# Kernel tuning notes

Hardware: AMD Instinct MI355X
Metric: run time of the kernel (lower is better)

The kernel has to match this reference:

```python
import jax, jax.numpy as jnp
import numpy as np

EPS = 1e-5
SLOPE = 0.2


def setup_inputs() -> dict:
    key = jax.random.key(0)
    ks = jax.random.split(key, 8)
    B, D, N = 8, 60, 1024
    dims = [(64, 120), (64, 64), (128, 64), (256, 128), (256, 512), (1024, 256)]
    inp = {"x": jax.random.normal(ks[0], (B, D, N), dtype=jnp.float32)}
    for i, (o, c) in enumerate(dims, 1):
        inp[f"w{i}"] = jax.random.normal(ks[i], (o, c), dtype=jnp.float32) / np.sqrt(c).astype(np.float32)
        inp[f"b{i}"] = jnp.zeros((o,), jnp.float32)
        inp[f"g{i}"] = jnp.ones((o,), jnp.float32)
        inp[f"be{i}"] = jnp.zeros((o,), jnp.float32)
    inp["k"] = 20
    return inp


def knn_idx(x, k):
    # x: [B, D, N] -> idx [B, N, k] of nearest neighbors (negative sq dist topk)
    inner = -2.0 * jnp.einsum('bdn,bdm->bnm', x, x)
    xx = jnp.sum(x * x, axis=1)  # [B, N]
    pd = -xx[:, :, None] - inner - xx[:, None, :]
    _, idx = jax.lax.top_k(pd, k)
    return idx


def get_graph_feature(x, k):
    # x: [B, D, N] -> [B, 2D, N, k]
    B, D, N = x.shape
    idx = knn_idx(x, k)  # [B, N, k]
    xt = jnp.transpose(x, (0, 2, 1))  # [B, N, D]
    nbr = xt[jnp.arange(B)[:, None, None], idx]  # [B, N, k, D]
    ctr = xt[:, :, None, :]  # [B, N, 1, D]
    feat = jnp.concatenate([nbr - ctr, jnp.broadcast_to(ctr, nbr.shape)], axis=-1)
    return jnp.transpose(feat, (0, 3, 1, 2))  # [B, 2D, N, k]


def lrelu(x):
    return jnp.where(x >= 0, x, SLOPE * x)


def bn(x, g, b, axes):
    # training-mode batch norm (biased variance), channel axis = 1
    m = jnp.mean(x, axis=axes, keepdims=True)
    v = jnp.mean((x - m) ** 2, axis=axes, keepdims=True)
    sh = [1] * x.ndim
    sh[1] = -1
    return (x - m) * jax.lax.rsqrt(v + EPS) * g.reshape(sh) + b.reshape(sh)


def conv2d1x1(x, w, b):
    return jnp.einsum('bcnk,oc->bonk', x, w) + b[None, :, None, None]


def conv1d1x1(x, w, b):
    return jnp.einsum('bcn,oc->bon', x, w) + b[None, :, None]


def reference(x, w1, b1, g1, be1, w2, b2, g2, be2, w3, b3, g3, be3,
              w4, b4, g4, be4, w5, b5, g5, be5, w6, b6, g6, be6, k):
    h = get_graph_feature(x, k)                             # [B,120,N,k]
    h = lrelu(bn(conv2d1x1(h, w1, b1), g1, be1, (0, 2, 3)))
    x1 = jnp.max(h, axis=-1)
    h = lrelu(bn(conv2d1x1(h, w2, b2), g2, be2, (0, 2, 3)))
    x2 = jnp.max(h, axis=-1)
    h = lrelu(bn(conv2d1x1(h, w3, b3), g3, be3, (0, 2, 3)))
    x3 = jnp.max(h, axis=-1)
    h = lrelu(bn(conv2d1x1(h, w4, b4), g4, be4, (0, 2, 3)))
    x4 = jnp.max(h, axis=-1)
    h = jnp.concatenate([x1, x2, x3, x4], axis=1)           # [B,512,N]
    h = lrelu(bn(conv1d1x1(h, w5, b5), g5, be5, (0, 2)))
    h = lrelu(bn(conv1d1x1(h, w6, b6), g6, be6, (0, 2)))
    return jnp.transpose(h, (0, 2, 1))                      # [B,N,emb_dims]
```

## Files before the change

kernel.cpp:

```cpp
#include <hip/hip_runtime.h>
#include <hip/hip_bf16.h>
#include <math.h>

#define B_ 8
#define D_ 60
#define N_ 1024
#define K_ 20
#define P1_ 8192
#define P2_ 163840

typedef __attribute__((ext_vector_type(8))) short bf16x8;
typedef __attribute__((ext_vector_type(4))) short bf16x4;
typedef __attribute__((ext_vector_type(4))) float f32x4;

__device__ inline float b2f(short s) { return __uint_as_float(((unsigned)(unsigned short)s) << 16); }
__device__ inline short f2b(float f) { __hip_bfloat16 h = __float2bfloat16(f); return *(short*)&h; }
__device__ inline unsigned fenc(float f) { unsigned b = __float_as_uint(f); return (b & 0x80000000u) ? ~b : (b | 0x80000000u); }
__device__ inline float fdec(unsigned k) { return __uint_as_float((k & 0x80000000u) ? (k ^ 0x80000000u) : ~k); }

#define OFF_IDX   0ull
#define OFF_XX    655360ull
#define OFF_STATS 688128ull
#define OFF_XT    720896ull
#define OFF_WB    1769472ull
#define OFF_XC    2662400ull
#define OFF_H5    11051008ull
#define OFF_H6    15245312ull
#define OFF_UV    32022528ull
#define OFF_XR1   36216832ull
#define OFF_XR2   38313984ull
#define OFF_XR3   40411136ull
#define OFF_XR4   44605440ull
#define OFF_H1    52994048ull
#define OFF_H2    73965568ull
#define OFF_H3    94937088ull
#define OFF_PART  136880128ull
#define OFF_PART2 139501568ull

#define WO1 0
#define WO2 8192
#define WO3 12288
#define WO4 20480
#define WO5 53248
#define WO6 184320

#define SO1 0
#define SO2 64
#define SO3 128
#define SO4 256
#define SO5 512
#define SO6 768
#define NCH_TOT 1792

__global__ __launch_bounds__(256) void k_xx(const float* __restrict__ x,
                                            float* __restrict__ xx) {
  int bn = blockIdx.x * 256 + threadIdx.x;
  int b = bn >> 10, n = bn & 1023;
  const float* xb = x + (size_t)b * D_ * N_ + n;
  float s = 0.f;
  for (int d = 0; d < D_; ++d) { float v = xb[(size_t)d * N_]; s += v * v; }
  xx[bn] = s;
}

__global__ __launch_bounds__(256) void k_pd(const float* __restrict__ x,
                                            const float* __restrict__ xx,
                                            float* __restrict__ pd) {
  __shared__ float lnn[D_][64];
  __shared__ float lmm[D_][128];
  int tid = threadIdx.x;
  int m0 = blockIdx.x * 128, n0 = blockIdx.y * 64, b = blockIdx.z;
  const float* xb = x + (size_t)b * D_ * N_;
  #pragma unroll
  for (int i = 0; i < 15; ++i) {
    int idx = tid + i * 256;
    int d = idx >> 6, col = idx & 63;
    lnn[d][col] = xb[(size_t)d * N_ + n0 + col];
  }
  #pragma unroll
  for (int i = 0; i < 30; ++i) {
    int idx = tid + i * 256;
    int d = idx >> 7, col = idx & 127;
    lmm[d][col] = xb[(size_t)d * N_ + m0 + col];
  }
  __syncthreads();
  int tn = tid >> 5, tm = tid & 31;
  float acc[8][4];
  #pragma unroll
  for (int i = 0; i < 8; ++i)
    #pragma unroll
    for (int j = 0; j < 4; ++j) acc[i][j] = 0.f;
  for (int d = 0; d < D_; ++d) {
    f32x4 mv  = *(const f32x4*)&lmm[d][tm * 4];
    f32x4 nva = *(const f32x4*)&lnn[d][tn * 8];
    f32x4 nvb = *(const f32x4*)&lnn[d][tn * 8 + 4];
    #pragma unroll
    for (int i = 0; i < 4; ++i)
      #pragma unroll
      for (int j = 0; j < 4; ++j) {
        acc[i][j]     = fmaf(nva[i], mv[j], acc[i][j]);
        acc[4 + i][j] = fmaf(nvb[i], mv[j], acc[4 + i][j]);
      }
  }
  const float* xxb = xx + b * 1024;
  f32x4 xxm = *(const f32x4*)(xxb + m0 + tm * 4);
  #pragma unroll
  for (int i = 0; i < 8; ++i) {
    int n = n0 + tn * 8 + i;
    float xxn = xxb[n];
    f32x4 o;
    #pragma unroll
    for (int j = 0; j < 4; ++j) o[j] = 2.f * acc[i][j] - xxn - xxm[j];
    *(f32x4*)(pd + ((size_t)(b * 1024 + n) * 1024) + m0 + tm * 4) = o;
  }
}

__global__ __launch_bounds__(256) void k_sel(const float* __restrict__ pd,
                                             int* __restrict__ idxb) {
  int tid = threadIdx.x;
  int wave = tid >> 6, lane = tid & 63;
  int bn = blockIdx.x * 4 + wave;
  const float* row = pd + (size_t)bn * 1024;
  int mbase = lane * 16;
  f32x4 r0 = *(const f32x4*)(row + mbase);
  f32x4 r1 = *(const f32x4*)(row + mbase + 4);
  f32x4 r2 = *(const f32x4*)(row + mbase + 8);
  f32x4 r3 = *(const f32x4*)(row + mbase + 12);
  float v[16];
  #pragma unroll
  for (int j = 0; j < 4; ++j) { v[j] = r0[j]; v[4 + j] = r1[j]; v[8 + j] = r2[j]; v[12 + j] = r3[j]; }
  int* outp = idxb + (size_t)bn * K_;
  for (int kk = 0; kk < K_; ++kk) {
    float bv = v[0]; int bj = 0;
    #pragma unroll
    for (int j = 1; j < 16; ++j)
      if (v[j] > bv) { bv = v[j]; bj = j; }
    int bi = mbase + bj;
    #pragma unroll
    for (int off = 1; off < 64; off <<= 1) {
      float ov = __shfl_xor(bv, off);
      int   oi = __shfl_xor(bi, off);
      if (ov > bv || (ov == bv && oi < bi)) { bv = ov; bi = oi; }
    }
    if (lane == 0) outp[kk] = bi;
    #pragma unroll
    for (int j = 0; j < 16; ++j)
      if (bi == mbase + j) v[j] = -INFINITY;
  }
}

__global__ __launch_bounds__(256) void k_xt(const float* __restrict__ x,
                                            short* __restrict__ xt) {
  int bn = blockIdx.x * 256 + threadIdx.x;
  int b = bn >> 10, n = bn & 1023;
  const float* xb = x + (size_t)b * D_ * N_ + n;
  short* row = xt + (size_t)bn * 64;
  for (int c = 0; c < 60; ++c) row[c] = f2b(xb[(size_t)c * N_]);
  row[60] = 0; row[61] = 0; row[62] = 0; row[63] = 0;
}

__global__ __launch_bounds__(256) void k_wuv(const float* __restrict__ w1,
                                             const float* __restrict__ b1,
                                             short* __restrict__ wuv,
                                             float* __restrict__ buv) {
  int t = blockIdx.x * 256 + threadIdx.x;
  int o = t >> 6, c = t & 63;
  float v = 0.f;
  if (o < 64) { if (c < 60) v = w1[o * 120 + c]; }
  else { int o2 = o - 64; if (c < 60) v = w1[o2 * 120 + 60 + c] - w1[o2 * 120 + c]; }
  wuv[t] = f2b(v);
  if (t < 128) buv[t] = (t < 64) ? 0.f : b1[t - 64];
}

__global__ __launch_bounds__(256) void k_wcvt(const float* __restrict__ w2,
                                              const float* __restrict__ w3,
                                              const float* __restrict__ w4,
                                              const float* __restrict__ w5,
                                              const float* __restrict__ w6,
                                              short* __restrict__ wbase) {
  int t = blockIdx.x * 256 + threadIdx.x;
  if (t < 4096) wbase[WO2 + t] = f2b(w2[t]);
  else if (t < 12288) wbase[WO3 + (t - 4096)] = f2b(w3[t - 4096]);
  else if (t < 45056) wbase[WO4 + (t - 12288)] = f2b(w4[t - 12288]);
  else if (t < 176128) wbase[WO5 + (t - 45056)] = f2b(w5[t - 45056]);
  else if (t < 438272) wbase[WO6 + (t - 176128)] = f2b(w6[t - 176128]);
}

template <int C>
__global__ __launch_bounds__(256) void k_act(short* __restrict__ h,
                                             const float* __restrict__ A,
                                             const float* __restrict__ Bp) {
  int t = blockIdx.x * 256 + threadIdx.x;
  int c0 = (t & (C / 8 - 1)) * 8;
  bf16x8 v = *(bf16x8*)(h + (size_t)t * 8);
  f32x4 a0 = *(const f32x4*)(A + c0), a1 = *(const f32x4*)(A + c0 + 4);
  f32x4 b0 = *(const f32x4*)(Bp + c0), b1 = *(const f32x4*)(Bp + c0 + 4);
  #pragma unroll
  for (int j = 0; j < 8; ++j) {
    float aj = j < 4 ? a0[j] : a1[j - 4];
    float bj = j < 4 ? b0[j] : b1[j - 4];
    float f = b2f(v[j]) * aj + bj;
    f = f >= 0.f ? f : 0.2f * f;
    v[j] = f2b(f);
  }
  *(bf16x8*)(h + (size_t)t * 8) = v;
}

template <int K, int COUT, bool APPLY, bool STATS, bool WMAX, bool HSTORE, bool F32OUT>
__global__ __launch_bounds__(256) void k_gemm(const short* __restrict__ in,
                                              const short* __restrict__ wb,
                                              const float* __restrict__ bias,
                                              const float* __restrict__ Ain,
                                              const float* __restrict__ Bin,
                                              float* __restrict__ part,
                                              short* __restrict__ out,
                                              unsigned* __restrict__ umax) {
  constexpr int PANEL = 64;
  constexpr int NPAN = K / PANEL;
  constexpr int CPR = PANEL / 8;
  constexpr int CSH = 3;
  constexpr int PK = PANEL + 8;
  constexpr int KS = PANEL / 32;
  constexpr int NX = COUT / 64;
  constexpr int SA = 128 * PK * 2;
  __shared__ __align__(16) char smem[SA + 64 * PK * 2 + 512];
  short* ldsA = (short*)smem;
  short* ldsW = (short*)(smem + SA);
  float* ls = (float*)(smem + SA + 64 * PK * 2);
  int tid = threadIdx.x;
  int w = tid >> 6, lane = tid & 63;
  int ln = lane & 15, quad = lane >> 4;
  int bid = blockIdx.y * NX + blockIdx.x;
  int tot = NX * gridDim.y;
  int gid = (bid & 7) * (tot >> 3) + (bid >> 3);
  int bxx = gid % NX;
  int rp = gid / NX;
  int co0 = bxx * 64;
  const short* srcA = in + (size_t)rp * 128 * K;
  const short* srcW = wb + (size_t)co0 * K;

  f32x4 acc[4][2];
  #pragma unroll
  for (int m = 0; m < 4; ++m)
    #pragma unroll
    for (int t = 0; t < 2; ++t) acc[m][t] = (f32x4){0.f, 0.f, 0.f, 0.f};

  for (int pan = 0; pan < NPAN; ++pan) {
    int kp = pan * PANEL;
    if (pan) __syncthreads();
    #pragma unroll
    for (int i = 0; i < CPR / 2; ++i) {
      int g = i * 256 + tid;
      int row = g >> CSH, c = g & (CPR - 1);
      bf16x8 v = *(const bf16x8*)(srcA + (size_t)row * K + kp + c * 8);
      if (APPLY) {
        f32x4 a0 = *(const f32x4*)(Ain + kp + c * 8);
        f32x4 a1 = *(const f32x4*)(Ain + kp + c * 8 + 4);
        f32x4 b0 = *(const f32x4*)(Bin + kp + c * 8);
        f32x4 b1 = *(const f32x4*)(Bin + kp + c * 8 + 4);
        #pragma unroll
        for (int j = 0; j < 8; ++j) {
          float aj = j < 4 ? a0[j] : a1[j - 4];
          float bj = j < 4 ? b0[j] : b1[j - 4];
          float f = b2f(v[j]) * aj + bj;
          f = f >= 0.f ? f : 0.2f * f;
          v[j] = f2b(f);
        }
      }
      *(bf16x8*)(ldsA + row * PK + c * 8) = v;
    }
    #pragma unroll
    for (int i = 0; i < CPR / 4; ++i) {
      int g = i * 256 + tid;
      int row = g >> CSH, c = g & (CPR - 1);
      *(bf16x8*)(ldsW + row * PK + c * 8) =
          *(const bf16x8*)(srcW + (size_t)row * K + kp + c * 8);
    }
    __syncthreads();
    #pragma unroll
    for (int ks = 0; ks < KS; ++ks) {
      bf16x8 a[4], bfr[2];
      #pragma unroll
      for (int m = 0; m < 4; ++m)
        a[m] = *(const bf16x8*)(ldsW + (m * 16 + ln) * PK + ks * 32 + quad * 8);
      #pragma unroll
      for (int t = 0; t < 2; ++t)
        bfr[t] = *(const bf16x8*)(ldsA + (w * 32 + t * 16 + ln) * PK + ks * 32 + quad * 8);
      #pragma unroll
      for (int m = 0; m < 4; ++m)
        #pragma unroll
        for (int t = 0; t < 2; ++t)
          acc[m][t] = __builtin_amdgcn_mfma_f32_16x16x32_bf16(a[m], bfr[t], acc[m][t], 0, 0, 0);
    }
  }
  #pragma unroll
  for (int m = 0; m < 4; ++m) {
    f32x4 bs = *(const f32x4*)(bias + co0 + m * 16 + quad * 4);
    #pragma unroll
    for (int t = 0; t < 2; ++t)
      #pragma unroll
      for (int r = 0; r < 4; ++r) acc[m][t][r] += bs[r];
  }
  if (HSTORE) {
    #pragma unroll
    for (int m = 0; m < 4; ++m)
      #pragma unroll
      for (int t = 0; t < 2; ++t) {
        int p = rp * 128 + w * 32 + t * 16 + ln;
        if (F32OUT) {
          *(f32x4*)((float*)out + (size_t)p * COUT + co0 + m * 16 + quad * 4) = acc[m][t];
        } else {
          bf16x4 o;
          #pragma unroll
          for (int r = 0; r < 4; ++r) o[r] = f2b(acc[m][t][r]);
          *(bf16x4*)(out + (size_t)p * COUT + co0 + m * 16 + quad * 4) = o;
        }
      }
  }
  if (STATS) {
    __syncthreads();
    if (tid < 128) ls[tid] = 0.f;
    __syncthreads();
    #pragma unroll
    for (int m = 0; m < 4; ++m)
      #pragma unroll
      for (int r = 0; r < 4; ++r) {
        float v0 = acc[m][0][r], v1 = acc[m][1][r];
        float s = v0 + v1, ss = v0 * v0 + v1 * v1;
        #pragma unroll
        for (int off = 1; off < 16; off <<= 1) {
          s += __shfl_xor(s, off); ss += __shfl_xor(ss, off);
        }
        if (ln == 0) {
          atomicAdd(&ls[m * 16 + quad * 4 + r], s);
          atomicAdd(&ls[64 + m * 16 + quad * 4 + r], ss);
        }
      }
    __syncthreads();
    if (tid < 128)
      part[((size_t)bxx * gridDim.y + rp) * 128 + tid] = ls[tid];
  }
  if (WMAX) {
    float* m32 = (float*)smem;
    #pragma unroll
    for (int half = 0; half < 2; ++half) {
      __syncthreads();
      if ((w >> 1) == half) {
        int lw = w & 1;
        #pragma unroll
        for (int m = 0; m < 4; ++m)
          #pragma unroll
          for (int t = 0; t < 2; ++t)
            *(f32x4*)(m32 + (size_t)(lw * 32 + t * 16 + ln) * 68 + m * 16 + quad * 4) = acc[m][t];
      }
      __syncthreads();
      int r0 = rp * 128 + half * 64;
      int pt0 = r0 / 20;
      int lpt = tid >> 6, col = tid & 63;
      int ptg = pt0 + lpt;
      int rs = ptg * 20 - r0, re = rs + 20;
      rs = rs < 0 ? 0 : rs;
      re = re > 64 ? 64 : re;
      if (rs < re) {
        float mv = -INFINITY;
        for (int r = rs; r < re; ++r) mv = fmaxf(mv, m32[r * 68 + col]);
        atomicMax(&umax[(size_t)ptg * COUT + co0 + col], fenc(mv));
      }
    }
  }
}

__global__ __launch_bounds__(256) void k_expand(const float* __restrict__ UVf,
                                                const int* __restrict__ idxb,
                                                short* __restrict__ h1,
                                                float* __restrict__ xr1,
                                                float* __restrict__ part) {
  int tid = threadIdx.x;
  int lp = tid >> 4;
  int c0 = (tid & 15) * 4;
  int pt = blockIdx.x * 16 + lp;
  int base = (pt >> 10) << 10;
  f32x4 V = *(const f32x4*)(UVf + (size_t)pt * 128 + 64 + c0);
  f32x4 sum = (f32x4){0.f, 0.f, 0.f, 0.f};
  f32x4 ssq = (f32x4){0.f, 0.f, 0.f, 0.f};
  f32x4 mx = (f32x4){-INFINITY, -INFINITY, -INFINITY, -INFINITY};
  const int* ip = idxb + (size_t)pt * K_;
  size_t hb = (size_t)pt * K_ * 64 + c0;
  for (int k = 0; k < K_; ++k) {
    int nb = base + ip[k];
    f32x4 U = *(const f32x4*)(UVf + (size_t)nb * 128 + c0);
    bf16x4 o;
    #pragma unroll
    for (int j = 0; j < 4; ++j) {
      float h = U[j] + V[j];
      mx[j] = fmaxf(mx[j], U[j]);
      sum[j] += h; ssq[j] += h * h;
      o[j] = f2b(h);
    }
    *(bf16x4*)(h1 + hb + (size_t)k * 64) = o;
  }
  f32x4 xo;
  #pragma unroll
  for (int j = 0; j < 4; ++j) xo[j] = mx[j] + V[j];
  *(f32x4*)(xr1 + (size_t)pt * 64 + c0) = xo;
  __shared__ float ls[2048];
  *(f32x4*)(ls + tid * 4) = sum;
  *(f32x4*)(ls + 1024 + tid * 4) = ssq;
  __syncthreads();
  if (tid < 32) {
    int cl = tid & 15;
    bool issq = tid >= 16;
    const float* src = ls + (issq ? 1024 : 0);
    f32x4 s = (f32x4){0.f, 0.f, 0.f, 0.f};
    #pragma unroll
    for (int g = 0; g < 16; ++g) {
      f32x4 v = *(const f32x4*)(src + (g * 16 + cl) * 4);
      s[0] += v[0]; s[1] += v[1]; s[2] += v[2]; s[3] += v[3];
    }
    *(f32x4*)(part + (size_t)blockIdx.x * 128 + (issq ? 64 : 0) + cl * 4) = s;
  }
}

__global__ __launch_bounds__(256) void k_red(const float* __restrict__ part, int NB,
                                             float* __restrict__ part2) {
  int cc = blockIdx.x, by = blockIdx.y;
  int tid = threadIdx.x;
  int rg = tid >> 5;
  int c4 = (tid & 31) * 4;
  int chunk = NB >> 5;
  const float* p = part + ((size_t)cc * NB + (size_t)by * chunk) * 128;
  f32x4 acc = (f32x4){0.f, 0.f, 0.f, 0.f};
  for (int r = rg; r < chunk; r += 8) {
    f32x4 v = *(const f32x4*)(p + (size_t)r * 128 + c4);
    acc[0] += v[0]; acc[1] += v[1]; acc[2] += v[2]; acc[3] += v[3];
  }
  __shared__ float lds[1024];
  *(f32x4*)(lds + tid * 4) = acc;
  __syncthreads();
  if (tid < 32) {
    f32x4 s = (f32x4){0.f, 0.f, 0.f, 0.f};
    #pragma unroll
    for (int g = 0; g < 8; ++g) {
      f32x4 v = *(const f32x4*)(lds + (g * 32 + tid) * 4);
      s[0] += v[0]; s[1] += v[1]; s[2] += v[2]; s[3] += v[3];
    }
    *(f32x4*)(part2 + ((size_t)cc * 32 + by) * 128 + tid * 4) = s;
  }
}

__global__ __launch_bounds__(256) void k_bnab(const float* __restrict__ part, int NB,
                                              const float* __restrict__ g,
                                              const float* __restrict__ be,
                                              float* __restrict__ A,
                                              float* __restrict__ Bp, float inv) {
  __shared__ float red[256];
  int tid = threadIdx.x;
  int j = tid & 127, h = tid >> 7;
  const float* p = part + (size_t)blockIdx.x * NB * 128;
  float s = 0.f;
  for (int bx = h; bx < NB; bx += 2) s += p[(size_t)bx * 128 + j];
  red[tid] = s;
  __syncthreads();
  if (tid < 128) red[tid] = red[tid] + red[tid + 128];
  __syncthreads();
  if (tid < 64) {
    int c = blockIdx.x * 64 + tid;
    float m = red[tid] * inv;
    float v = red[64 + tid] * inv - m * m;
    float a = g[c] * rsqrtf(v + 1e-5f);
    A[c] = a; Bp[c] = be[c] - m * a;
  }
}

__global__ __launch_bounds__(256) void k_xcat(const float* __restrict__ xr1,
                                              const unsigned* __restrict__ xr2,
                                              const unsigned* __restrict__ xr3,
                                              const unsigned* __restrict__ xr4,
                                              const float* __restrict__ A,
                                              const float* __restrict__ Bp,
                                              short* __restrict__ xcat) {
  int t = blockIdx.x * 256 + threadIdx.x;
  int p = t >> 7, cq = t & 127;
  int c0 = cq * 4;
  f32x4 v;
  if (c0 < 64) {
    v = *(const f32x4*)(xr1 + (size_t)p * 64 + c0);
  } else {
    const unsigned* src; int cc;
    if (c0 < 128)      { src = xr2 + (size_t)p * 64;  cc = c0 - 64; }
    else if (c0 < 256) { src = xr3 + (size_t)p * 128; cc = c0 - 128; }
    else               { src = xr4 + (size_t)p * 256; cc = c0 - 256; }
    #pragma unroll
    for (int j = 0; j < 4; ++j) v[j] = fdec(src[cc + j]);
  }
  f32x4 a = *(const f32x4*)(A + c0);
  f32x4 b = *(const f32x4*)(Bp + c0);
  bf16x4 o;
  #pragma unroll
  for (int j = 0; j < 4; ++j) {
    float f = v[j] * a[j] + b[j];
    f = f >= 0.f ? f : 0.2f * f;
    o[j] = f2b(f);
  }
  *(bf16x4*)(xcat + (size_t)p * 512 + c0) = o;
}

__global__ __launch_bounds__(256) void k_apply_out(const short* __restrict__ h,
                                                   const float* __restrict__ A,
                                                   const float* __restrict__ Bp,
                                                   float* __restrict__ out) {
  int t = blockIdx.x * 256 + threadIdx.x;
  int c0 = (t & 255) * 4;
  f32x4 a = *(const f32x4*)(A + c0);
  f32x4 b = *(const f32x4*)(Bp + c0);
  bf16x4 v = *(const bf16x4*)(h + (size_t)t * 4);
  f32x4 o;
  #pragma unroll
  for (int r = 0; r < 4; ++r) {
    float f = b2f(v[r]) * a[r] + b[r];
    o[r] = f >= 0.f ? f : 0.2f * f;
  }
  *(f32x4*)(out + (size_t)t * 4) = o;
}

extern "C" void kernel_launch(void* const* d_in, const int* in_sizes, int n_in,
                              void* d_out, int out_size, void* d_ws, size_t ws_size,
                              hipStream_t stream) {
  const float* x   = (const float*)d_in[0];
  const float* w1  = (const float*)d_in[1];
  const float* b1  = (const float*)d_in[2];
  const float* g1  = (const float*)d_in[3];
  const float* be1 = (const float*)d_in[4];
  const float* w2  = (const float*)d_in[5];
  const float* b2  = (const float*)d_in[6];
  const float* g2  = (const float*)d_in[7];
  const float* be2 = (const float*)d_in[8];
  const float* w3  = (const float*)d_in[9];
  const float* b3  = (const float*)d_in[10];
  const float* g3  = (const float*)d_in[11];
  const float* be3 = (const float*)d_in[12];
  const float* w4  = (const float*)d_in[13];
  const float* b4  = (const float*)d_in[14];
  const float* g4  = (const float*)d_in[15];
  const float* be4 = (const float*)d_in[16];
  const float* w5  = (const float*)d_in[17];
  const float* b5  = (const float*)d_in[18];
  const float* g5  = (const float*)d_in[19];
  const float* be5 = (const float*)d_in[20];
  const float* w6  = (const float*)d_in[21];
  const float* b6  = (const float*)d_in[22];
  const float* g6  = (const float*)d_in[23];
  const float* be6 = (const float*)d_in[24];
  float* out = (float*)d_out;
  char* ws = (char*)d_ws;

  int*      idxb = (int*)(ws + OFF_IDX);
  float*    xx   = (float*)(ws + OFF_XX);
  float*    Aall = (float*)(ws + OFF_STATS);
  float*    Ball = Aall + NCH_TOT;
  float*    buv  = Ball + NCH_TOT;
  short*    xt   = (short*)(ws + OFF_XT);
  short*    wbb  = (short*)(ws + OFF_WB);
  short*    xcat = (short*)(ws + OFF_XC);
  short*    h5   = (short*)(ws + OFF_H5);
  short*    h6   = (short*)(ws + OFF_H6);
  float*    UVf  = (float*)(ws + OFF_UV);
  float*    xr1  = (float*)(ws + OFF_XR1);
  unsigned* xr2  = (unsigned*)(ws + OFF_XR2);
  unsigned* xr3  = (unsigned*)(ws + OFF_XR3);
  unsigned* xr4  = (unsigned*)(ws + OFF_XR4);
  short*    h1   = (short*)(ws + OFF_H1);
  short*    h2   = (short*)(ws + OFF_H2);
  short*    h3   = (short*)(ws + OFF_H3);
  float*    pd    = (float*)(ws + OFF_H3);
  float*    part  = (float*)(ws + OFF_PART);
  float*    part2 = (float*)(ws + OFF_PART2);

  hipMemsetAsync(ws + OFF_XR2, 0, 2097152ull + 4194304ull + 8388608ull, stream);

  k_xx <<<P1_ / 256, 256, 0, stream>>>(x, xx);
  k_pd <<<dim3(8, 16, 8), 256, 0, stream>>>(x, xx, pd);
  k_sel<<<P1_ / 4, 256, 0, stream>>>(pd, idxb);
  k_xt <<<P1_ / 256, 256, 0, stream>>>(x, xt);
  k_wuv<<<32, 256, 0, stream>>>(w1, b1, wbb + WO1, buv);
  k_wcvt<<<1712, 256, 0, stream>>>(w2, w3, w4, w5, w6, wbb);

  k_gemm<64, 128, false, false, false, true, true><<<dim3(2, 64), 256, 0, stream>>>(
      xt, wbb + WO1, buv, nullptr, nullptr, nullptr, (short*)UVf, nullptr);
  k_expand<<<P1_ / 16, 256, 0, stream>>>(UVf, idxb, h1, xr1, part);
  k_red <<<dim3(1, 32), 256, 0, stream>>>(part, P1_ / 16, part2);
  k_bnab<<<1, 256, 0, stream>>>(part2, 32, g1, be1, Aall + SO1, Ball + SO1, 1.f / P2_);

  k_gemm<64, 64, true, true, true, true, false><<<dim3(1, P2_ / 128), 256, 0, stream>>>(
      h1, wbb + WO2, b2, Aall + SO1, Ball + SO1, part, h2, xr2);
  k_red <<<dim3(1, 32), 256, 0, stream>>>(part, P2_ / 128, part2);
  k_bnab<<<1, 256, 0, stream>>>(part2, 32, g2, be2, Aall + SO2, Ball + SO2, 1.f / P2_);

  k_gemm<64, 128, true, true, true, true, false><<<dim3(2, P2_ / 128), 256, 0, stream>>>(
      h2, wbb + WO3, b3, Aall + SO2, Ball + SO2, part, h3, xr3);
  k_red <<<dim3(2, 32), 256, 0, stream>>>(part, P2_ / 128, part2);
  k_bnab<<<2, 256, 0, stream>>>(part2, 32, g3, be3, Aall + SO3, Ball + SO3, 1.f / P2_);

  k_act<128><<<P2_ * 128 / 2048, 256, 0, stream>>>(h3, Aall + SO3, Ball + SO3);

  k_gemm<128, 256, false, true, true, false, false><<<dim3(4, P2_ / 128), 256, 0, stream>>>(
      h3, wbb + WO4, b4, nullptr, nullptr, part, nullptr, xr4);
  k_red <<<dim3(4, 32), 256, 0, stream>>>(part, P2_ / 128, part2);
  k_bnab<<<4, 256, 0, stream>>>(part2, 32, g4, be4, Aall + SO4, Ball + SO4, 1.f / P2_);

  k_xcat<<<P1_ * 128 / 256, 256, 0, stream>>>(xr1, xr2, xr3, xr4, Aall, Ball, xcat);

  k_gemm<512, 256, false, true, false, true, false><<<dim3(4, P1_ / 128), 256, 0, stream>>>(
      xcat, wbb + WO5, b5, nullptr, nullptr, part, h5, nullptr);
  k_bnab<<<4, 256, 0, stream>>>(part, P1_ / 128, g5, be5, Aall + SO5, Ball + SO5, 1.f / P1_);

  k_act<256><<<P1_ * 256 / 2048, 256, 0, stream>>>(h5, Aall + SO5, Ball + SO5);

  k_gemm<256, 1024, false, true, false, true, false><<<dim3(16, P1_ / 128), 256, 0, stream>>>(
      h5, wbb + WO6, b6, nullptr, nullptr, part, h6, nullptr);
  k_bnab<<<16, 256, 0, stream>>>(part, P1_ / 128, g6, be6, Aall + SO6, Ball + SO6, 1.f / P1_);
  k_apply_out<<<P1_ * 256 / 256, 256, 0, stream>>>(h6, Aall + SO6, Ball + SO6, out);

  (void)in_sizes; (void)n_in; (void)out_size; (void)ws_size;
}
```

Before: 436.5 us.

## Restructure GEMM with register double-buffering, multi-tile blocks, and shuffle-based max

Rewrites the shared GEMM kernel so each block handles several row tiles and output-channel tiles. It prefetches the next A/W tiles into registers while computing the current one, and keeps W resident in LDS when it fits. Per-wave BN statistics now go directly to global partials, and the neighbor max is a shuffle reduction instead of an LDS staging pass. The separate layer-3 activation kernel is removed and folded into layer-4's input load (APPLY). This cuts launch count, LDS round trips and redundant weight loads, at the cost of more registers and more partial-stat reduction work.

```diff
diff --git a/kernel.cpp b/kernel.cpp
--- a/kernel.cpp
+++ b/kernel.cpp
@@ -35,7 +35,7 @@
 #define OFF_H2    73965568ull
 #define OFF_H3    94937088ull
 #define OFF_PART  136880128ull
-#define OFF_PART2 139501568ull
+#define OFF_PART2 149463040ull
 
 #define WO1 0
 #define WO2 8192
@@ -205,7 +205,7 @@
   *(bf16x8*)(h + (size_t)t * 8) = v;
 }
 
-template <int K, int COUT, bool APPLY, bool STATS, bool WMAX, bool HSTORE, bool F32OUT>
+template <int K, int COUT, int NR, int NCO, bool APPLY, bool STATS, bool WMAX, bool HSTORE, bool F32OUT>
 __global__ __launch_bounds__(256) void k_gemm(const short* __restrict__ in,
                                               const short* __restrict__ wb,
                                               const float* __restrict__ bias,
@@ -214,156 +214,202 @@
                                               float* __restrict__ part,
                                               short* __restrict__ out,
                                               unsigned* __restrict__ umax) {
-  constexpr int PANEL = 64;
-  constexpr int NPAN = K / PANEL;
-  constexpr int CPR = PANEL / 8;
-  constexpr int CSH = 3;
-  constexpr int PK = PANEL + 8;
-  constexpr int KS = PANEL / 32;
-  constexpr int NX = COUT / 64;
-  constexpr int SA = 128 * PK * 2;
-  __shared__ __align__(16) char smem[SA + 64 * PK * 2 + 512];
-  short* ldsA = (short*)smem;
-  short* ldsW = (short*)(smem + SA);
-  float* ls = (float*)(smem + SA + 64 * PK * 2);
+  constexpr int NKP = (K > 128) ? (K / 64) : 1;
+  constexpr int KA  = (K > 128) ? 64 : K;
+  constexpr int PKA = KA + 8;
+  constexpr int PKW = KA + 8;
+  constexpr bool W_RES = (NKP == 1) && (NCO <= 2);
+  constexpr int WROWS = W_RES ? NCO * 64 : 64;
+  constexpr int NIT = NR * NCO * NKP;
+  constexpr int ACPR = KA / 8;
+  constexpr int ACSH = (ACPR == 16) ? 4 : 3;
+  constexpr int ALOADS = (128 * KA) / (256 * 8);
+  constexpr int WLOADS = (WROWS * KA) / (256 * 8);
+  constexpr int NSTEP = (W_RES && NCO == 2) ? 2 : 1;
+  constexpr int KS = KA / 32;
+
+  __shared__ short ldsA[128 * PKA];
+  __shared__ short ldsW[WROWS * PKW];
+
   int tid = threadIdx.x;
   int w = tid >> 6, lane = tid & 63;
   int ln = lane & 15, quad = lane >> 4;
-  int bid = blockIdx.y * NX + blockIdx.x;
-  int tot = NX * gridDim.y;
+  int bid = blockIdx.y * gridDim.x + blockIdx.x;
+  int tot = gridDim.x * gridDim.y;
   int gid = (bid & 7) * (tot >> 3) + (bid >> 3);
-  int bxx = gid % NX;
-  int rp = gid / NX;
-  int co0 = bxx * 64;
-  const short* srcA = in + (size_t)rp * 128 * K;
-  const short* srcW = wb + (size_t)co0 * K;
+  int bxx = gid % gridDim.x;
+  int rp = gid / gridDim.x;
+
+  auto stgA = [](int i2) { return (NKP > 1) || ((i2 % (NCO > 0 ? NCO : 1)) == 0); };
+  auto stgW = [](int i2) { return !W_RES || i2 == 0; };
+
+  auto issueA = [&](int i2, bf16x8* dst) {
+    const int r_ = i2 / (NCO * NKP), kp_ = i2 % NKP;
+    const short* src = in + (size_t)((rp * NR + r_) * 128) * K + kp_ * 64;
+    #pragma unroll
+    for (int l = 0; l < ALOADS; ++l) {
+      int gI = l * 256 + tid, rowI = gI >> ACSH, cI = gI & (ACPR - 1);
+      dst[l] = *(const bf16x8*)(src + (size_t)rowI * K + cI * 8);
+    }
+  };
+  auto issueW = [&](int i2, bf16x8* dst) {
+    const int kp_ = i2 % NKP, co_ = (i2 / NKP) % NCO;
+    const short* src = wb + (size_t)(bxx * NCO * 64 + (W_RES ? 0 : co_ * 64)) * K + kp_ * 64;
+    #pragma unroll
+    for (int l = 0; l < WLOADS; ++l) {
+      int gI = l * 256 + tid, rowI = gI >> ACSH, cI = gI & (ACPR - 1);
+      dst[l] = *(const bf16x8*)(src + (size_t)rowI * K + cI * 8);
+    }
+  };
+  auto writeA = [&](int i2, bf16x8* srcR) {
+    const int kp_ = i2 % NKP;
+    #pragma unroll
+    for (int l = 0; l < ALOADS; ++l) {
+      int gI = l * 256 + tid, rowI = gI >> ACSH, cI = gI & (ACPR - 1);
+      bf16x8 v = srcR[l];
+      if (APPLY) {
+        int kc = kp_ * 64 + cI * 8;
+        f32x4 a0 = *(const f32x4*)(Ain + kc), a1 = *(const f32x4*)(Ain + kc + 4);
+        f32x4 b0 = *(const f32x4*)(Bin + kc), b1 = *(const f32x4*)(Bin + kc + 4);
+        #pragma unroll
+        for (int jj = 0; jj < 8; ++jj) {
+          float aj = jj < 4 ? a0[jj] : a1[jj - 4];
+          float bj = jj < 4 ? b0[jj] : b1[jj - 4];
+          float f = b2f(v[jj]) * aj + bj;
+          f = f >= 0.f ? f : 0.2f * f;
+          v[jj] = f2b(f);
+        }
+      }
+      *(bf16x8*)(ldsA + rowI * PKA + cI * 8) = v;
+    }
+  };
+  auto writeW = [&](bf16x8* srcR) {
+    #pragma unroll
+    for (int l = 0; l < WLOADS; ++l) {
+      int gI = l * 256 + tid, rowI = gI >> ACSH, cI = gI & (ACPR - 1);
+      *(bf16x8*)(ldsW + rowI * PKW + cI * 8) = srcR[l];
+    }
+  };
+
+  bf16x8 rAa[ALOADS], rAb[ALOADS], rWa[WLOADS], rWb[WLOADS];
+  issueA(0, rAa);
+  issueW(0, rWa);
+  writeA(0, rAa);
+  writeW(rWa);
+  if (NSTEP < NIT) {
+    if (stgA(NSTEP)) issueA(NSTEP, rAb);
+    if (stgW(NSTEP)) issueW(NSTEP, rWb);
+  }
+  __syncthreads();
 
   f32x4 acc[4][2];
   #pragma unroll
-  for (int m = 0; m < 4; ++m)
-    #pragma unroll
-    for (int t = 0; t < 2; ++t) acc[m][t] = (f32x4){0.f, 0.f, 0.f, 0.f};
-
-  for (int pan = 0; pan < NPAN; ++pan) {
-    int kp = pan * PANEL;
-    if (pan) __syncthreads();
-    #pragma unroll
-    for (int i = 0; i < CPR / 2; ++i) {
-      int g = i * 256 + tid;
-      int row = g >> CSH, c = g & (CPR - 1);
-      bf16x8 v = *(const bf16x8*)(srcA + (size_t)row * K + kp + c * 8);
-      if (APPLY) {
-        f32x4 a0 = *(const f32x4*)(Ain + kp + c * 8);
-        f32x4 a1 = *(const f32x4*)(Ain + kp + c * 8 + 4);
-        f32x4 b0 = *(const f32x4*)(Bin + kp + c * 8);
-        f32x4 b1 = *(const f32x4*)(Bin + kp + c * 8 + 4);
-        #pragma unroll
-        for (int j = 0; j < 8; ++j) {
-          float aj = j < 4 ? a0[j] : a1[j - 4];
-          float bj = j < 4 ? b0[j] : b1[j - 4];
-          float f = b2f(v[j]) * aj + bj;
-          f = f >= 0.f ? f : 0.2f * f;
-          v[j] = f2b(f);
-        }
-      }
-      *(bf16x8*)(ldsA + row * PK + c * 8) = v;
-    }
-    #pragma unroll
-    for (int i = 0; i < CPR / 4; ++i) {
-      int g = i * 256 + tid;
-      int row = g >> CSH, c = g & (CPR - 1);
-      *(bf16x8*)(ldsW + row * PK + c * 8) =
-          *(const bf16x8*)(srcW + (size_t)row * K + kp + c * 8);
-    }
-    __syncthreads();
-    #pragma unroll
-    for (int ks = 0; ks < KS; ++ks) {
-      bf16x8 a[4], bfr[2];
+  for (int i = 0; i < NIT; ++i) {
+    if (i && (i % NSTEP) == 0) {
+      const int e = i / NSTEP;
+      __syncthreads();
+      if (stgA(i)) writeA(i, (e & 1) ? rAb : rAa);
+      if (stgW(i)) writeW((e & 1) ? rWb : rWa);
+      if (i + NSTEP < NIT) {
+        if (stgA(i + NSTEP)) issueA(i + NSTEP, (e & 1) ? rAa : rAb);
+        if (stgW(i + NSTEP)) issueW(i + NSTEP, (e & 1) ? rWa : rWb);
+      }
+      __syncthreads();
+    }
+    if ((i % NKP) == 0) {
       #pragma unroll
       for (int m = 0; m < 4; ++m)
-        a[m] = *(const bf16x8*)(ldsW + (m * 16 + ln) * PK + ks * 32 + quad * 8);
+        #pragma unroll
+        for (int t = 0; t < 2; ++t) acc[m][t] = (f32x4){0.f, 0.f, 0.f, 0.f};
+    }
+    {
+      const int wbase = W_RES ? (((i / NKP) % NCO) * 64) : 0;
       #pragma unroll
-      for (int t = 0; t < 2; ++t)
-        bfr[t] = *(const bf16x8*)(ldsA + (w * 32 + t * 16 + ln) * PK + ks * 32 + quad * 8);
-      #pragma unroll
-      for (int m = 0; m < 4; ++m)
+      for (int ks = 0; ks < KS; ++ks) {
+        bf16x8 fw[4], fa[2];
+        #pragma unroll
+        for (int m = 0; m < 4; ++m)
+          fw[m] = *(const bf16x8*)(ldsW + (wbase + m * 16 + ln) * PKW + ks * 32 + quad * 8);
         #pragma unroll
         for (int t = 0; t < 2; ++t)
-          acc[m][t] = __builtin_amdgcn_mfma_f32_16x16x32_bf16(a[m], bfr[t], acc[m][t], 0, 0, 0);
-    }
-  }
-  #pragma unroll
-  for (int m = 0; m < 4; ++m) {
-    f32x4 bs = *(const f32x4*)(bias + co0 + m * 16 + quad * 4);
-    #pragma unroll
-    for (int t = 0; t < 2; ++t)
-      #pragma unroll
-      for (int r = 0; r < 4; ++r) acc[m][t][r] += bs[r];
-  }
-  if (HSTORE) {
-    #pragma unroll
-    for (int m = 0; m < 4; ++m)
-      #pragma unroll
-      for (int t = 0; t < 2; ++t) {
-        int p = rp * 128 + w * 32 + t * 16 + ln;
-        if (F32OUT) {
-          *(f32x4*)((float*)out + (size_t)p * COUT + co0 + m * 16 + quad * 4) = acc[m][t];
-        } else {
-          bf16x4 o;
-          #pragma unroll
-          for (int r = 0; r < 4; ++r) o[r] = f2b(acc[m][t][r]);
-          *(bf16x4*)(out + (size_t)p * COUT + co0 + m * 16 + quad * 4) = o;
-        }
-      }
-  }
-  if (STATS) {
-    __syncthreads();
-    if (tid < 128) ls[tid] = 0.f;
-    __syncthreads();
-    #pragma unroll
-    for (int m = 0; m < 4; ++m)
-      #pragma unroll
-      for (int r = 0; r < 4; ++r) {
-        float v0 = acc[m][0][r], v1 = acc[m][1][r];
-        float s = v0 + v1, ss = v0 * v0 + v1 * v1;
-        #pragma unroll
-        for (int off = 1; off < 16; off <<= 1) {
-          s += __shfl_xor(s, off); ss += __shfl_xor(ss, off);
-        }
-        if (ln == 0) {
-          atomicAdd(&ls[m * 16 + quad * 4 + r], s);
-          atomicAdd(&ls[64 + m * 16 + quad * 4 + r], ss);
-        }
-      }
-    __syncthreads();
-    if (tid < 128)
-      part[((size_t)bxx * gridDim.y + rp) * 128 + tid] = ls[tid];
-  }
-  if (WMAX) {
-    float* m32 = (float*)smem;
-    #pragma unroll
-    for (int half = 0; half < 2; ++half) {
-      __syncthreads();
-      if ((w >> 1) == half) {
-        int lw = w & 1;
+          fa[t] = *(const bf16x8*)(ldsA + (w * 32 + t * 16 + ln) * PKA + ks * 32 + quad * 8);
         #pragma unroll
         for (int m = 0; m < 4; ++m)
           #pragma unroll
           for (int t = 0; t < 2; ++t)
-            *(f32x4*)(m32 + (size_t)(lw * 32 + t * 16 + ln) * 68 + m * 16 + quad * 4) = acc[m][t];
-      }
-      __syncthreads();
-      int r0 = rp * 128 + half * 64;
-      int pt0 = r0 / 20;
-      int lpt = tid >> 6, col = tid & 63;
-      int ptg = pt0 + lpt;
-      int rs = ptg * 20 - r0, re = rs + 20;
-      rs = rs < 0 ? 0 : rs;
-      re = re > 64 ? 64 : re;
-      if (rs < re) {
-        float mv = -INFINITY;
-        for (int r = rs; r < re; ++r) mv = fmaxf(mv, m32[r * 68 + col]);
-        atomicMax(&umax[(size_t)ptg * COUT + co0 + col], fenc(mv));
+            acc[m][t] = __builtin_amdgcn_mfma_f32_16x16x32_bf16(fw[m], fa[t], acc[m][t], 0, 0, 0);
+      }
+    }
+    if ((i % NKP) == (NKP - 1)) {
+      const int r_  = i / (NCO * NKP);
+      const int co_ = (i / NKP) % NCO;
+      const int cog = bxx * NCO + co_;
+      const int co0 = cog * 64;
+      #pragma unroll
+      for (int m = 0; m < 4; ++m) {
+        f32x4 bs = *(const f32x4*)(bias + co0 + m * 16 + quad * 4);
+        #pragma unroll
+        for (int t = 0; t < 2; ++t)
+          #pragma unroll
+          for (int j = 0; j < 4; ++j) acc[m][t][j] += bs[j];
+      }
+      const int prow = (rp * NR + r_) * 128 + w * 32;
+      if (HSTORE) {
+        #pragma unroll
+        for (int m = 0; m < 4; ++m)
+          #pragma unroll
+          for (int t = 0; t < 2; ++t) {
+            int p = prow + t * 16 + ln;
+            if (F32OUT) {
+              *(f32x4*)((float*)out + (size_t)p * COUT + co0 + m * 16 + quad * 4) = acc[m][t];
+            } else {
+              bf16x4 o;
+              #pragma unroll
+              for (int jr = 0; jr < 4; ++jr) o[jr] = f2b(acc[m][t][jr]);
+              *(bf16x4*)(out + (size_t)p * COUT + co0 + m * 16 + quad * 4) = o;
+            }
+          }
+      }
+      if (STATS) {
+        size_t key = ((size_t)cog * (gridDim.y * NR) + (size_t)(rp * NR + r_)) * 4 + w;
+        float* pp = part + key * 128;
+        #pragma unroll
+        for (int m = 0; m < 4; ++m)
+          #pragma unroll
+          for (int j = 0; j < 4; ++j) {
+            float v0 = acc[m][0][j], v1 = acc[m][1][j];
+            float s = v0 + v1, ss = v0 * v0 + v1 * v1;
+            #pragma unroll
+            for (int off = 1; off < 16; off <<= 1) {
+              s += __shfl_xor(s, off); ss += __shfl_xor(ss, off);
+            }
+            if (ln == 0) {
+              pp[m * 16 + quad * 4 + j] = s;
+              pp[64 + m * 16 + quad * 4 + j] = ss;
+            }
+          }
+      }
+      if (WMAX) {
+        #pragma unroll
+        for (int t = 0; t < 2; ++t) {
+          int row = prow + t * 16 + ln;
+          int g = row / 20;
+          bool lead = (ln == 0) || (row - g * 20 == 0);
+          int og1 = __shfl_xor(g, 1), og2 = __shfl_xor(g, 2);
+          int og4 = __shfl_xor(g, 4), og8 = __shfl_xor(g, 8);
+          #pragma unroll
+          for (int m = 0; m < 4; ++m)
+            #pragma unroll
+            for (int j = 0; j < 4; ++j) {
+              float v = acc[m][t][j];
+              float ov;
+              ov = __shfl_xor(v, 1); if (og1 == g && ov > v) v = ov;
+              ov = __shfl_xor(v, 2); if (og2 == g && ov > v) v = ov;
+              ov = __shfl_xor(v, 4); if (og4 == g && ov > v) v = ov;
+              ov = __shfl_xor(v, 8); if (og8 == g && ov > v) v = ov;
+              if (lead) atomicMax(&umax[(size_t)g * COUT + co0 + m * 16 + quad * 4 + j], fenc(v));
+            }
+        }
       }
     }
   }
@@ -584,40 +630,38 @@
   k_wuv<<<32, 256, 0, stream>>>(w1, b1, wbb + WO1, buv);
   k_wcvt<<<1712, 256, 0, stream>>>(w2, w3, w4, w5, w6, wbb);
 
-  k_gemm<64, 128, false, false, false, true, true><<<dim3(2, 64), 256, 0, stream>>>(
+  k_gemm<64, 128, 1, 1, false, false, false, true, true><<<dim3(2, 64), 256, 0, stream>>>(
       xt, wbb + WO1, buv, nullptr, nullptr, nullptr, (short*)UVf, nullptr);
   k_expand<<<P1_ / 16, 256, 0, stream>>>(UVf, idxb, h1, xr1, part);
   k_red <<<dim3(1, 32), 256, 0, stream>>>(part, P1_ / 16, part2);
   k_bnab<<<1, 256, 0, stream>>>(part2, 32, g1, be1, Aall + SO1, Ball + SO1, 1.f / P2_);
 
-  k_gemm<64, 64, true, true, true, true, false><<<dim3(1, P2_ / 128), 256, 0, stream>>>(
+  k_gemm<64, 64, 2, 1, true, true, true, true, false><<<dim3(1, 640), 256, 0, stream>>>(
       h1, wbb + WO2, b2, Aall + SO1, Ball + SO1, part, h2, xr2);
-  k_red <<<dim3(1, 32), 256, 0, stream>>>(part, P2_ / 128, part2);
+  k_red <<<dim3(1, 32), 256, 0, stream>>>(part, 5120, part2);
   k_bnab<<<1, 256, 0, stream>>>(part2, 32, g2, be2, Aall + SO2, Ball + SO2, 1.f / P2_);
 
-  k_gemm<64, 128, true, true, true, true, false><<<dim3(2, P2_ / 128), 256, 0, stream>>>(
+  k_gemm<64, 128, 2, 2, true, true, true, true, false><<<dim3(1, 640), 256, 0, stream>>>(
       h2, wbb + WO3, b3, Aall + SO2, Ball + SO2, part, h3, xr3);
-  k_red <<<dim3(2, 32), 256, 0, stream>>>(part, P2_ / 128, part2);
+  k_red <<<dim3(2, 32), 256, 0, stream>>>(part, 5120, part2);
   k_bnab<<<2, 256, 0, stream>>>(part2, 32, g3, be3, Aall + SO3, Ball + SO3, 1.f / P2_);
 
-  k_act<128><<<P2_ * 128 / 2048, 256, 0, stream>>>(h3, Aall + SO3, Ball + SO3);
-
-  k_gemm<128, 256, false, true, true, false, false><<<dim3(4, P2_ / 128), 256, 0, stream>>>(
-      h3, wbb + WO4, b4, nullptr, nullptr, part, nullptr, xr4);
-  k_red <<<dim3(4, 32), 256, 0, stream>>>(part, P2_ / 128, part2);
+  k_gemm<128, 256, 1, 4, true, true, true, false, false><<<dim3(1, 1280), 256, 0, stream>>>(
+      h3, wbb + WO4, b4, Aall + SO3, Ball + SO3, part, nullptr, xr4);
+  k_red <<<dim3(4, 32), 256, 0, stream>>>(part, 5120, part2);
   k_bnab<<<4, 256, 0, stream>>>(part2, 32, g4, be4, Aall + SO4, Ball + SO4, 1.f / P2_);
 
   k_xcat<<<P1_ * 128 / 256, 256, 0, stream>>>(xr1, xr2, xr3, xr4, Aall, Ball, xcat);
 
-  k_gemm<512, 256, false, true, false, true, false><<<dim3(4, P1_ / 128), 256, 0, stream>>>(
+  k_gemm<512, 256, 1, 1, false, true, false, true, false><<<dim3(4, 64), 256, 0, stream>>>(
       xcat, wbb + WO5, b5, nullptr, nullptr, part, h5, nullptr);
-  k_bnab<<<4, 256, 0, stream>>>(part, P1_ / 128, g5, be5, Aall + SO5, Ball + SO5, 1.f / P1_);
+  k_bnab<<<4, 256, 0, stream>>>(part, 256, g5, be5, Aall + SO5, Ball + SO5, 1.f / P1_);
 
   k_act<256><<<P1_ * 256 / 2048, 256, 0, stream>>>(h5, Aall + SO5, Ball + SO5);
 
-  k_gemm<256, 1024, false, true, false, true, false><<<dim3(16, P1_ / 128), 256, 0, stream>>>(
+  k_gemm<256, 1024, 2, 1, false, true, false, true, false><<<dim3(16, 32), 256, 0, stream>>>(
       h5, wbb + WO6, b6, nullptr, nullptr, part, h6, nullptr);
-  k_bnab<<<16, 256, 0, stream>>>(part, P1_ / 128, g6, be6, Aall + SO6, Ball + SO6, 1.f / P1_);
+  k_bnab<<<16, 256, 0, stream>>>(part, 256, g6, be6, Aall + SO6, Ball + SO6, 1.f / P1_);
   k_apply_out<<<P1_ * 256 / 256, 256, 0, stream>>>(h6, Aall + SO6, Ball + SO6, out);
 
   (void)in_sizes; (void)n_in; (void)out_size; (void)ws_size;
```

Result: slower. 587.1 us (+34.5%).

## Move layer 2/3 stats and k-max from GEMM epilogue into separate reduction kernel

Applied to the files above, without the earlier changes.

For layers 2 and 3, the GEMM no longer computes BN statistics or the atomic neighbor max. A new k_maxh kernel re-reads the stored bf16 output and computes the per-point max plus per-channel sum and sum-of-squares, written as float partials. This drops the k_red pass, the atomics, and part of the memset. The cost is an extra full read of h2 and h3. The LDS row padding also shrinks from 8 to 4 shorts, and the stats scratch is allocated only when needed.

```diff
diff --git a/kernel.cpp b/kernel.cpp
--- a/kernel.cpp
+++ b/kernel.cpp
@@ -205,6 +205,53 @@
   *(bf16x8*)(h + (size_t)t * 8) = v;
 }
 
+template <int C>
+__global__ __launch_bounds__(256) void k_maxh(const short* __restrict__ h,
+                                              float* __restrict__ xrf,
+                                              float* __restrict__ part) {
+  constexpr int TPP = C / 8;
+  constexpr int PTS = 256 / TPP;
+  __shared__ float lsS[256 * 8];
+  __shared__ float lsQ[256 * 8];
+  int tid = threadIdx.x;
+  int lp = tid / TPP;
+  int c0 = (tid % TPP) * 8;
+  int pt = blockIdx.x * PTS + lp;
+  const short* hp = h + (size_t)pt * K_ * C + c0;
+  float mx[8], sm[8], sq[8];
+  #pragma unroll
+  for (int j = 0; j < 8; ++j) { mx[j] = -INFINITY; sm[j] = 0.f; sq[j] = 0.f; }
+  for (int k = 0; k < K_; ++k) {
+    bf16x8 v = *(const bf16x8*)(hp + (size_t)k * C);
+    #pragma unroll
+    for (int j = 0; j < 8; ++j) {
+      float f = b2f(v[j]);
+      mx[j] = fmaxf(mx[j], f);
+      sm[j] += f; sq[j] += f * f;
+    }
+  }
+  f32x4 m0, m1;
+  #pragma unroll
+  for (int j = 0; j < 4; ++j) { m0[j] = mx[j]; m1[j] = mx[4 + j]; }
+  *(f32x4*)(xrf + (size_t)pt * C + c0) = m0;
+  *(f32x4*)(xrf + (size_t)pt * C + c0 + 4) = m1;
+  #pragma unroll
+  for (int j = 0; j < 8; ++j) { lsS[tid * 8 + j] = sm[j]; lsQ[tid * 8 + j] = sq[j]; }
+  __syncthreads();
+  if (tid < C) {
+    int ci = tid >> 3, e = tid & 7;
+    float s = 0.f, q = 0.f;
+    #pragma unroll
+    for (int p = 0; p < PTS; ++p) {
+      s += lsS[(p * TPP + ci) * 8 + e];
+      q += lsQ[(p * TPP + ci) * 8 + e];
+    }
+    size_t base = ((size_t)(tid >> 6) * gridDim.x + blockIdx.x) * 128;
+    part[base + (tid & 63)] = s;
+    part[base + 64 + (tid & 63)] = q;
+  }
+}
+
 template <int K, int COUT, bool APPLY, bool STATS, bool WMAX, bool HSTORE, bool F32OUT>
 __global__ __launch_bounds__(256) void k_gemm(const short* __restrict__ in,
                                               const short* __restrict__ wb,
@@ -218,11 +265,12 @@
   constexpr int NPAN = K / PANEL;
   constexpr int CPR = PANEL / 8;
   constexpr int CSH = 3;
-  constexpr int PK = PANEL + 8;
+  constexpr int PK = PANEL + 4;
   constexpr int KS = PANEL / 32;
   constexpr int NX = COUT / 64;
   constexpr int SA = 128 * PK * 2;
-  __shared__ __align__(16) char smem[SA + 64 * PK * 2 + 512];
+  constexpr int LSB = STATS ? 512 : 0;
+  __shared__ __align__(16) char smem[SA + 64 * PK * 2 + LSB];
   short* ldsA = (short*)smem;
   short* ldsW = (short*)(smem + SA);
   float* ls = (float*)(smem + SA + 64 * PK * 2);
@@ -472,8 +520,8 @@
 }
 
 __global__ __launch_bounds__(256) void k_xcat(const float* __restrict__ xr1,
-                                              const unsigned* __restrict__ xr2,
-                                              const unsigned* __restrict__ xr3,
+                                              const float* __restrict__ xr2f,
+                                              const float* __restrict__ xr3f,
                                               const unsigned* __restrict__ xr4,
                                               const float* __restrict__ A,
                                               const float* __restrict__ Bp,
@@ -484,11 +532,13 @@
   f32x4 v;
   if (c0 < 64) {
     v = *(const f32x4*)(xr1 + (size_t)p * 64 + c0);
+  } else if (c0 < 128) {
+    v = *(const f32x4*)(xr2f + (size_t)p * 64 + (c0 - 64));
+  } else if (c0 < 256) {
+    v = *(const f32x4*)(xr3f + (size_t)p * 128 + (c0 - 128));
   } else {
-    const unsigned* src; int cc;
-    if (c0 < 128)      { src = xr2 + (size_t)p * 64;  cc = c0 - 64; }
-    else if (c0 < 256) { src = xr3 + (size_t)p * 128; cc = c0 - 128; }
-    else               { src = xr4 + (size_t)p * 256; cc = c0 - 256; }
+    const unsigned* src = xr4 + (size_t)p * 256;
+    int cc = c0 - 256;
     #pragma unroll
     for (int j = 0; j < 4; ++j) v[j] = fdec(src[cc + j]);
   }
@@ -565,8 +615,8 @@
   short*    h6   = (short*)(ws + OFF_H6);
   float*    UVf  = (float*)(ws + OFF_UV);
   float*    xr1  = (float*)(ws + OFF_XR1);
-  unsigned* xr2  = (unsigned*)(ws + OFF_XR2);
-  unsigned* xr3  = (unsigned*)(ws + OFF_XR3);
+  float*    xr2f = (float*)(ws + OFF_XR2);
+  float*    xr3f = (float*)(ws + OFF_XR3);
   unsigned* xr4  = (unsigned*)(ws + OFF_XR4);
   short*    h1   = (short*)(ws + OFF_H1);
   short*    h2   = (short*)(ws + OFF_H2);
@@ -575,7 +625,7 @@
   float*    part  = (float*)(ws + OFF_PART);
   float*    part2 = (float*)(ws + OFF_PART2);
 
-  hipMemsetAsync(ws + OFF_XR2, 0, 2097152ull + 4194304ull + 8388608ull, stream);
+  hipMemsetAsync(ws + OFF_XR4, 0, 8388608ull, stream);
 
   k_xx <<<P1_ / 256, 256, 0, stream>>>(x, xx);
   k_pd <<<dim3(8, 16, 8), 256, 0, stream>>>(x, xx, pd);
@@ -590,15 +640,15 @@
   k_red <<<dim3(1, 32), 256, 0, stream>>>(part, P1_ / 16, part2);
   k_bnab<<<1, 256, 0, stream>>>(part2, 32, g1, be1, Aall + SO1, Ball + SO1, 1.f / P2_);
 
-  k_gemm<64, 64, true, true, true, true, false><<<dim3(1, P2_ / 128), 256, 0, stream>>>(
-      h1, wbb + WO2, b2, Aall + SO1, Ball + SO1, part, h2, xr2);
-  k_red <<<dim3(1, 32), 256, 0, stream>>>(part, P2_ / 128, part2);
-  k_bnab<<<1, 256, 0, stream>>>(part2, 32, g2, be2, Aall + SO2, Ball + SO2, 1.f / P2_);
-
-  k_gemm<64, 128, true, true, true, true, false><<<dim3(2, P2_ / 128), 256, 0, stream>>>(
-      h2, wbb + WO3, b3, Aall + SO2, Ball + SO2, part, h3, xr3);
-  k_red <<<dim3(2, 32), 256, 0, stream>>>(part, P2_ / 128, part2);
-  k_bnab<<<2, 256, 0, stream>>>(part2, 32, g3, be3, Aall + SO3, Ball + SO3, 1.f / P2_);
+  k_gemm<64, 64, true, false, false, true, false><<<dim3(1, P2_ / 128), 256, 0, stream>>>(
+      h1, wbb + WO2, b2, Aall + SO1, Ball + SO1, nullptr, h2, nullptr);
+  k_maxh<64><<<P1_ / 32, 256, 0, stream>>>(h2, xr2f, part);
+  k_bnab<<<1, 256, 0, stream>>>(part, P1_ / 32, g2, be2, Aall + SO2, Ball + SO2, 1.f / P2_);
+
+  k_gemm<64, 128, true, false, false, true, false><<<dim3(2, P2_ / 128), 256, 0, stream>>>(
+      h2, wbb + WO3, b3, Aall + SO2, Ball + SO2, nullptr, h3, nullptr);
+  k_maxh<128><<<P1_ / 16, 256, 0, stream>>>(h3, xr3f, part);
+  k_bnab<<<2, 256, 0, stream>>>(part, P1_ / 16, g3, be3, Aall + SO3, Ball + SO3, 1.f / P2_);
 
   k_act<128><<<P2_ * 128 / 2048, 256, 0, stream>>>(h3, Aall + SO3, Ball + SO3);
 
@@ -607,7 +657,7 @@
   k_red <<<dim3(4, 32), 256, 0, stream>>>(part, P2_ / 128, part2);
   k_bnab<<<4, 256, 0, stream>>>(part2, 32, g4, be4, Aall + SO4, Ball + SO4, 1.f / P2_);
 
-  k_xcat<<<P1_ * 128 / 256, 256, 0, stream>>>(xr1, xr2, xr3, xr4, Aall, Ball, xcat);
+  k_xcat<<<P1_ * 128 / 256, 256, 0, stream>>>(xr1, xr2f, xr3f, xr4, Aall, Ball, xcat);
 
   k_gemm<512, 256, false, true, false, true, false><<<dim3(4, P1_ / 128), 256, 0, stream>>>(
       xcat, wbb + WO5, b5, nullptr, nullptr, part, h5, nullptr);
```

After: 590.3 us. 35.2% more time.
